# Performance work log

Measured on AMD Instinct MI355X. Metric: run time of the kernel, lower is better.

## Reference

```python
import jax, jax.numpy as jnp
import numpy as np

B, T, DIN, H, NOUT = 256, 512, 64, 512, 128


def setup_inputs() -> dict:
    key = jax.random.key(0)
    ks = jax.random.split(key, 11)
    s = 1.0 / np.sqrt(H)  # PyTorch GRU init scale
    inp = {"x": jax.random.normal(ks[0], (B, T, DIN), dtype=jnp.float32)}
    # layer 0 (input DIN), layer 1 (input H); gate order: r, z, n
    inp["w_ih0"] = jax.random.uniform(ks[1], (3 * H, DIN), minval=-s, maxval=s)
    inp["w_hh0"] = jax.random.uniform(ks[2], (3 * H, H), minval=-s, maxval=s)
    inp["b_ih0"] = jax.random.uniform(ks[3], (3 * H,), minval=-s, maxval=s)
    inp["b_hh0"] = jax.random.uniform(ks[4], (3 * H,), minval=-s, maxval=s)
    inp["w_ih1"] = jax.random.uniform(ks[5], (3 * H, H), minval=-s, maxval=s)
    inp["w_hh1"] = jax.random.uniform(ks[6], (3 * H, H), minval=-s, maxval=s)
    inp["b_ih1"] = jax.random.uniform(ks[7], (3 * H,), minval=-s, maxval=s)
    inp["b_hh1"] = jax.random.uniform(ks[8], (3 * H,), minval=-s, maxval=s)
    inp["w_fc"] = jax.random.uniform(ks[9], (NOUT, H), minval=-s, maxval=s)
    inp["b_fc"] = jax.random.uniform(ks[10], (NOUT,), minval=-s, maxval=s)
    return inp


def _gru_layer(x_seq, w_ih, w_hh, b_ih, b_hh):
    # x_seq: [B, T, Din] -> hidden trajectory [B, T, H]
    xg = jnp.einsum('btd,gd->btg', x_seq, w_ih) + b_ih  # [B, T, 3H], precomputed input gates
    h0 = jnp.zeros((x_seq.shape[0], w_hh.shape[1]), dtype=x_seq.dtype)

    def step(h, xg_t):
        hg = h @ w_hh.T + b_hh
        xr, xz, xn = jnp.split(xg_t, 3, axis=-1)
        hr, hz, hn = jnp.split(hg, 3, axis=-1)
        r = jax.nn.sigmoid(xr + hr)
        z = jax.nn.sigmoid(xz + hz)
        n = jnp.tanh(xn + r * hn)
        h_new = (1.0 - z) * n + z * h
        return h_new, h_new

    _, hs = jax.lax.scan(step, h0, jnp.swapaxes(xg, 0, 1))  # [T, B, H]
    return jnp.swapaxes(hs, 0, 1)


def reference(x, w_ih0, w_hh0, b_ih0, b_hh0, w_ih1, w_hh1, b_ih1, b_hh1, w_fc, b_fc):
    h1 = _gru_layer(x, w_ih0, w_hh0, b_ih0, b_hh0)   # [B, T, H]
    h2 = _gru_layer(h1, w_ih1, w_hh1, b_ih1, b_hh1)  # [B, T, H]
    last = h2[:, -1, :]                               # [B, H]
    return last @ w_fc.T + b_fc                       # [B, NOUT]
```

## Files before the change

### kernel.cpp

```cpp
#include <hip/hip_runtime.h>
#include <math.h>

typedef unsigned short u16;
typedef __attribute__((ext_vector_type(8))) short s8v;
typedef __attribute__((ext_vector_type(4))) float f4v;
typedef __attribute__((ext_vector_type(4))) int   i4v;

constexpr int kB    = 256;
constexpr int kT    = 512;
constexpr int kDIN  = 64;
constexpr int kH    = 512;
constexpr int kG3   = 1536;
constexpr int kNOUT = 128;
constexpr int kPlane = 8 * 2 * 16 * 512;
constexpr int kXStep = 16 * 2 * 512;

#define MFMA16 __builtin_amdgcn_mfma_f32_16x16x32_bf16

__device__ __forceinline__ u16 f2bf(float f) {
  union { float f; unsigned u; } v; v.f = f;
  unsigned r = (v.u + 0x7FFFu + ((v.u >> 16) & 1u)) >> 16;
  return (u16)r;
}
__device__ __forceinline__ float fsig(float x) {
  x = fminf(fmaxf(x, -30.f), 30.f);
  float e = __expf(-x);
  return __fdividef(1.f, 1.f + e);
}
__device__ __forceinline__ float ftanh(float x) {
  x = fminf(fmaxf(x, -15.f), 15.f);
  float e = __expf(-2.f * x);
  return __fdividef(1.f - e, 1.f + e);
}

__device__ __forceinline__ void load16_nw(const u16* base, i4v a[16]) {
  asm volatile(
      "global_load_dwordx4 %0, %16, off sc0 sc1\n\t"
      "global_load_dwordx4 %1, %16, off offset:1024 sc0 sc1\n\t"
      "global_load_dwordx4 %2, %16, off offset:2048 sc0 sc1\n\t"
      "global_load_dwordx4 %3, %16, off offset:3072 sc0 sc1\n\t"
      "global_load_dwordx4 %4, %17, off sc0 sc1\n\t"
      "global_load_dwordx4 %5, %17, off offset:1024 sc0 sc1\n\t"
      "global_load_dwordx4 %6, %17, off offset:2048 sc0 sc1\n\t"
      "global_load_dwordx4 %7, %17, off offset:3072 sc0 sc1\n\t"
      "global_load_dwordx4 %8, %18, off sc0 sc1\n\t"
      "global_load_dwordx4 %9, %18, off offset:1024 sc0 sc1\n\t"
      "global_load_dwordx4 %10, %18, off offset:2048 sc0 sc1\n\t"
      "global_load_dwordx4 %11, %18, off offset:3072 sc0 sc1\n\t"
      "global_load_dwordx4 %12, %19, off sc0 sc1\n\t"
      "global_load_dwordx4 %13, %19, off offset:1024 sc0 sc1\n\t"
      "global_load_dwordx4 %14, %19, off offset:2048 sc0 sc1\n\t"
      "global_load_dwordx4 %15, %19, off offset:3072 sc0 sc1"
      : "=&v"(a[0]), "=&v"(a[1]), "=&v"(a[2]), "=&v"(a[3]),
        "=&v"(a[4]), "=&v"(a[5]), "=&v"(a[6]), "=&v"(a[7]),
        "=&v"(a[8]), "=&v"(a[9]), "=&v"(a[10]), "=&v"(a[11]),
        "=&v"(a[12]), "=&v"(a[13]), "=&v"(a[14]), "=&v"(a[15])
      : "v"(base), "v"(base + 4 * 512), "v"(base + 8 * 512), "v"(base + 12 * 512)
      : "memory");
}

__device__ __forceinline__ void store_h_l0(
    u16* p0, u16* p1, u16* p2, u16* p3,
    u16* q0, u16* q1, u16* q2, u16* q3,
    unsigned v0, unsigned v1, unsigned v2, unsigned v3) {
  asm volatile(
      "global_store_short %0, %8, off sc0 sc1\n\t"
      "global_store_short %1, %9, off sc0 sc1\n\t"
      "global_store_short %2, %10, off sc0 sc1\n\t"
      "global_store_short %3, %11, off sc0 sc1\n\t"
      "global_store_short %4, %8, off\n\t"
      "global_store_short %5, %9, off\n\t"
      "global_store_short %6, %10, off\n\t"
      "global_store_short %7, %11, off\n\t"
      "s_waitcnt vmcnt(4)"
      :: "v"(p0), "v"(p1), "v"(p2), "v"(p3),
         "v"(q0), "v"(q1), "v"(q2), "v"(q3),
         "v"(v0), "v"(v1), "v"(v2), "v"(v3)
      : "memory");
}
__device__ __forceinline__ void store_h_l1(
    u16* p0, u16* p1, u16* p2, u16* p3,
    unsigned v0, unsigned v1, unsigned v2, unsigned v3) {
  asm volatile(
      "global_store_short %0, %4, off sc0 sc1\n\t"
      "global_store_short %1, %5, off sc0 sc1\n\t"
      "global_store_short %2, %6, off sc0 sc1\n\t"
      "global_store_short %3, %7, off sc0 sc1\n\t"
      "s_waitcnt vmcnt(0)"
      :: "v"(p0), "v"(p1), "v"(p2), "v"(p3),
         "v"(v0), "v"(v1), "v"(v2), "v"(v3)
      : "memory");
}

__global__ void build_wslab(const float* __restrict__ w, u16* __restrict__ d) {
  int idx  = blockIdx.x * 256 + threadIdx.x;
  int lane = idx & 63, fg = idx >> 6;
  int jt = fg / 96, f = fg % 96;
  int nt = f >> 4, kt = f & 15;
  int g = nt >> 1, u = nt & 1;
  int row = g * 512 + jt * 32 + u * 16 + (lane & 15);
  int k0  = kt * 32 + (lane >> 4) * 8;
  const float* src = w + (size_t)row * 512 + k0;
  u16* dst = d + ((size_t)fg) * 512 + lane * 8;
#pragma unroll
  for (int i = 0; i < 8; i++) dst[i] = f2bf(src[i]);
}

__global__ void build_wslab_ih0(const float* __restrict__ w, u16* __restrict__ d) {
  int idx  = blockIdx.x * 256 + threadIdx.x;
  int lane = idx & 63, fg = idx >> 6;
  int jt = fg / 12, f = fg % 12;
  int nt = f >> 1, kt = f & 1;
  int g = nt >> 1, u = nt & 1;
  int row = g * 512 + jt * 32 + u * 16 + (lane & 15);
  int k0  = kt * 32 + (lane >> 4) * 8;
  const float* src = w + (size_t)row * kDIN + k0;
  u16* dst = d + ((size_t)fg) * 512 + lane * 8;
#pragma unroll
  for (int i = 0; i < 8; i++) dst[i] = f2bf(src[i]);
}

__global__ void build_xplane(const float* __restrict__ x, u16* __restrict__ d) {
  int idx  = blockIdx.x * 256 + threadIdx.x;
  int lane = idx & 63, fg = idx >> 6;
  int kt = fg & 1, m = (fg >> 1) & 15, T = fg >> 5;
  int b  = m * 16 + (lane & 15);
  int k0 = kt * 32 + (lane >> 4) * 8;
  const float* src = x + ((size_t)b * kT + T) * kDIN + k0;
  u16* dst = d + ((size_t)fg) * 512 + lane * 8;
#pragma unroll
  for (int i = 0; i < 8; i++) dst[i] = f2bf(src[i]);
}

__global__ __launch_bounds__(256, 1)
void rec_fused(int c, int TC, int nc, unsigned bar_base16, unsigned* bar,
               const u16* __restrict__ xpl,
               const u16* __restrict__ slab0hh, const u16* __restrict__ slab0ih,
               const u16* __restrict__ slab1hh, const u16* __restrict__ slab1ih,
               const float* __restrict__ bih0, const float* __restrict__ bhh0,
               const float* __restrict__ bih1, const float* __restrict__ bhh1,
               u16* __restrict__ h1pl, u16* __restrict__ hbuf,
               float* __restrict__ carry) {
  __shared__ u16 ldsw[96 * 512];

  const int bid   = blockIdx.x;
  const int layer = bid >> 7;
  const int lb    = bid & 127;
  const int jt    = lb & 15, bt = lb >> 4;
  const int cc    = (layer == 0) ? c : c - 1;
  const bool active = (cc >= 0 && cc < nc);

  unsigned* mybar = bar + (size_t)(layer * 8 + bt) * 64;

  if (!active) {
    if (threadIdx.x == 0)
      __hip_atomic_fetch_add(mybar, (unsigned)TC, __ATOMIC_RELAXED,
                             __HIP_MEMORY_SCOPE_AGENT);
    return;
  }

  const int tid   = threadIdx.x;
  const int wv    = tid >> 6, lane = tid & 63;
  const int mt    = wv >> 1, u = wv & 1;
  const int jl    = lane & 15;
  const int jg    = jt * 32 + u * 16 + jl;
  const int mrow  = (lane >> 4) * 4;
  const int bbase = bt * 32 + mt * 16 + mrow;

  const size_t cons_off = ((size_t)((bt * 2 + mt) * 16)) * 512 + lane * 8;
  const size_t prod_off = ((size_t)((bt * 2 + mt) * 16 + jt)) * 512 +
                          (size_t)(16 * (u * 2 + (jl >> 3))) * 8 + (jl & 7);
  float* mycarry = carry + (size_t)layer * kB * kH;

  if (layer == 0) {
    s8v bh[3][16];
    {
      const u16* base = slab0hh + (size_t)jt * 96 * 512 + (size_t)lane * 8;
#pragma unroll
      for (int g = 0; g < 3; ++g)
#pragma unroll
        for (int kt = 0; kt < 16; ++kt)
          bh[g][kt] = *(const s8v*)(base + (size_t)((g * 2 + u) * 16 + kt) * 512);
    }
    s8v bx[3][2];
    {
      const u16* base = slab0ih + (size_t)jt * 12 * 512 + (size_t)lane * 8;
#pragma unroll
      for (int g = 0; g < 3; ++g)
#pragma unroll
        for (int kt = 0; kt < 2; ++kt)
          bx[g][kt] = *(const s8v*)(base + (size_t)((g * 2 + u) * 2 + kt) * 512);
    }
    const float br  = bih0[jg] + bhh0[jg];
    const float bz  = bih0[512 + jg] + bhh0[512 + jg];
    const float bni = bih0[1024 + jg], bnh = bhh0[1024 + jg];

    float hp[4];
#pragma unroll
    for (int r = 0; r < 4; ++r)
      hp[r] = mycarry[(size_t)(bbase + r) * 512 + jg];

    const size_t xoff = (size_t)((bt * 2 + mt) * 2) * 512 + (size_t)lane * 8;
    const u16* xb0 = xpl + (size_t)(cc * TC) * kXStep + xoff;
    s8v ax0 = *(const s8v*)xb0;
    s8v ax1 = *(const s8v*)(xb0 + 512);

    for (int t = 0; t < TC; ++t) {
      if (tid == 0) {
        unsigned tgt = bar_base16 + 16u * (unsigned)t;
        int guard = 0;
        while (__hip_atomic_load(mybar, __ATOMIC_RELAXED,
                                 __HIP_MEMORY_SCOPE_AGENT) < tgt
               && ++guard < (1 << 21))
          __builtin_amdgcn_s_sleep(1);
      }
      __syncthreads();

      i4v a[16];
      load16_nw(hbuf + (size_t)(t & 1) * kPlane + cons_off, a);

      const f4v z4 = {0.f, 0.f, 0.f, 0.f};
      f4v acc0, acc1, acc2, acc2x;
      acc0  = MFMA16(ax0, bx[0][0], z4, 0, 0, 0);
      acc0  = MFMA16(ax1, bx[0][1], acc0, 0, 0, 0);
      acc1  = MFMA16(ax0, bx[1][0], z4, 0, 0, 0);
      acc1  = MFMA16(ax1, bx[1][1], acc1, 0, 0, 0);
      acc2x = MFMA16(ax0, bx[2][0], z4, 0, 0, 0);
      acc2x = MFMA16(ax1, bx[2][1], acc2x, 0, 0, 0);
      acc2  = z4;
      asm volatile("s_waitcnt vmcnt(0)" ::: "memory");
      __builtin_amdgcn_sched_barrier(0);
#pragma unroll
      for (int kt = 0; kt < 16; ++kt) {
        const s8v av = __builtin_bit_cast(s8v, a[kt]);
        acc0 = MFMA16(av, bh[0][kt], acc0, 0, 0, 0);
        acc1 = MFMA16(av, bh[1][kt], acc1, 0, 0, 0);
        acc2 = MFMA16(av, bh[2][kt], acc2, 0, 0, 0);
      }

      unsigned hv[4];
#pragma unroll
      for (int r = 0; r < 4; ++r) {
        float rr = fsig(acc0[r] + br);
        float zz = fsig(acc1[r] + bz);
        float nn = ftanh(acc2x[r] + bni + rr * (acc2[r] + bnh));
        float hn = (1.f - zz) * nn + zz * hp[r];
        hp[r] = hn;
        hv[r] = f2bf(hn);
      }

      u16* pb = hbuf + (size_t)((t + 1) & 1) * kPlane + prod_off;
      u16* qb = h1pl + (size_t)((cc & 1) * TC + t) * kPlane + prod_off;
      store_h_l0(pb + (size_t)(mrow + 0) * 8, pb + (size_t)(mrow + 1) * 8,
                 pb + (size_t)(mrow + 2) * 8, pb + (size_t)(mrow + 3) * 8,
                 qb + (size_t)(mrow + 0) * 8, qb + (size_t)(mrow + 1) * 8,
                 qb + (size_t)(mrow + 2) * 8, qb + (size_t)(mrow + 3) * 8,
                 hv[0], hv[1], hv[2], hv[3]);
      __syncthreads();
      if (tid == 0)
        __hip_atomic_fetch_add(mybar, 1u, __ATOMIC_RELAXED,
                               __HIP_MEMORY_SCOPE_AGENT);
      if (t + 1 < TC) {
        const u16* xb = xpl + (size_t)(cc * TC + t + 1) * kXStep + xoff;
        ax0 = *(const s8v*)xb;
        ax1 = *(const s8v*)(xb + 512);
      }
    }
#pragma unroll
    for (int r = 0; r < 4; ++r)
      mycarry[(size_t)(bbase + r) * 512 + jg] = hp[r];
  } else {
    {
      const u16* src = slab1ih + (size_t)jt * 96 * 512;
      for (int i = tid; i < 96 * 512 / 8; i += 256)
        *(s8v*)&ldsw[i * 8] = *(const s8v*)&src[i * 8];
    }
    s8v bh[3][16];
    {
      const u16* base = slab1hh + (size_t)jt * 96 * 512 + (size_t)lane * 8;
#pragma unroll
      for (int g = 0; g < 3; ++g)
#pragma unroll
        for (int kt = 0; kt < 16; ++kt)
          bh[g][kt] = *(const s8v*)(base + (size_t)((g * 2 + u) * 16 + kt) * 512);
    }
    const float br  = bih1[jg] + bhh1[jg];
    const float bz  = bih1[512 + jg] + bhh1[512 + jg];
    const float bni = bih1[1024 + jg], bnh = bhh1[1024 + jg];

    float hp[4];
#pragma unroll
    for (int r = 0; r < 4; ++r)
      hp[r] = mycarry[(size_t)(bbase + r) * 512 + jg];

    const u16* h1base = h1pl + (size_t)((cc & 1) * TC) * kPlane + cons_off;
    i4v a1[16];
    load16_nw(h1base, a1);

    for (int t = 0; t < TC; ++t) {
      if (tid == 0) {
        unsigned tgt = bar_base16 + 16u * (unsigned)t;
        int guard = 0;
        while (__hip_atomic_load(mybar, __ATOMIC_RELAXED,
                                 __HIP_MEMORY_SCOPE_AGENT) < tgt
               && ++guard < (1 << 21))
          __builtin_amdgcn_s_sleep(1);
      }
      __syncthreads();

      i4v a2[16];
      load16_nw(hbuf + (size_t)(2 + (t & 1)) * kPlane + cons_off, a2);
      asm volatile("s_waitcnt vmcnt(16)" ::: "memory");
      __builtin_amdgcn_sched_barrier(0);

      const f4v z4 = {0.f, 0.f, 0.f, 0.f};
      f4v acc0 = z4, acc1 = z4, acc2 = z4, acc2x = z4;
#pragma unroll
      for (int kt = 0; kt < 16; ++kt) {
        const s8v b0 = *(const s8v*)&ldsw[(size_t)((0 + u) * 16 + kt) * 512 + lane * 8];
        const s8v b1 = *(const s8v*)&ldsw[(size_t)((2 + u) * 16 + kt) * 512 + lane * 8];
        const s8v b2 = *(const s8v*)&ldsw[(size_t)((4 + u) * 16 + kt) * 512 + lane * 8];
        const s8v av = __builtin_bit_cast(s8v, a1[kt]);
        acc0  = MFMA16(av, b0, acc0, 0, 0, 0);
        acc1  = MFMA16(av, b1, acc1, 0, 0, 0);
        acc2x = MFMA16(av, b2, acc2x, 0, 0, 0);
      }
      asm volatile("s_waitcnt vmcnt(0)" ::: "memory");
      __builtin_amdgcn_sched_barrier(0);
#pragma unroll
      for (int kt = 0; kt < 16; ++kt) {
        const s8v av = __builtin_bit_cast(s8v, a2[kt]);
        acc0 = MFMA16(av, bh[0][kt], acc0, 0, 0, 0);
        acc1 = MFMA16(av, bh[1][kt], acc1, 0, 0, 0);
        acc2 = MFMA16(av, bh[2][kt], acc2, 0, 0, 0);
      }

      unsigned hv[4];
#pragma unroll
      for (int r = 0; r < 4; ++r) {
        float rr = fsig(acc0[r] + br);
        float zz = fsig(acc1[r] + bz);
        float nn = ftanh(acc2x[r] + bni + rr * (acc2[r] + bnh));
        float hn = (1.f - zz) * nn + zz * hp[r];
        hp[r] = hn;
        hv[r] = f2bf(hn);
      }

      u16* pb = hbuf + (size_t)(2 + ((t + 1) & 1)) * kPlane + prod_off;
      store_h_l1(pb + (size_t)(mrow + 0) * 8, pb + (size_t)(mrow + 1) * 8,
                 pb + (size_t)(mrow + 2) * 8, pb + (size_t)(mrow + 3) * 8,
                 hv[0], hv[1], hv[2], hv[3]);
      if (t + 1 < TC)
        load16_nw(h1base + (size_t)(t + 1) * kPlane, a1);
      __syncthreads();
      if (tid == 0)
        __hip_atomic_fetch_add(mybar, 1u, __ATOMIC_RELAXED,
                               __HIP_MEMORY_SCOPE_AGENT);
    }
#pragma unroll
    for (int r = 0; r < 4; ++r)
      mycarry[(size_t)(bbase + r) * 512 + jg] = hp[r];
  }
}

__global__ __launch_bounds__(128)
void fc_kernel(const float* __restrict__ h, const float* __restrict__ wfc,
               const float* __restrict__ bfc, float* __restrict__ out) {
  const int b = blockIdx.x;
  const int n = threadIdx.x;
  const float* hrow = h + (size_t)b * kH;
  const float* wrow = wfc + (size_t)n * kH;
  float acc = 0.f;
#pragma unroll 4
  for (int k = 0; k < kH; k += 4) {
    const float4 hv = *(const float4*)&hrow[k];
    const float4 wv = *(const float4*)&wrow[k];
    acc = fmaf(hv.x, wv.x, acc); acc = fmaf(hv.y, wv.y, acc);
    acc = fmaf(hv.z, wv.z, acc); acc = fmaf(hv.w, wv.w, acc);
  }
  out[(size_t)b * kNOUT + n] = acc + bfc[n];
}

extern "C" void kernel_launch(void* const* d_in, const int* in_sizes, int n_in,
                              void* d_out, int out_size, void* d_ws, size_t ws_size,
                              hipStream_t stream) {
  const float* x     = (const float*)d_in[0];
  const float* w_ih0 = (const float*)d_in[1];
  const float* w_hh0 = (const float*)d_in[2];
  const float* b_ih0 = (const float*)d_in[3];
  const float* b_hh0 = (const float*)d_in[4];
  const float* w_ih1 = (const float*)d_in[5];
  const float* w_hh1 = (const float*)d_in[6];
  const float* b_ih1 = (const float*)d_in[7];
  const float* b_hh1 = (const float*)d_in[8];
  const float* w_fc  = (const float*)d_in[9];
  const float* b_fc  = (const float*)d_in[10];
  float* out = (float*)d_out;

  auto need = [](int tc) -> size_t {
    size_t s = 0;
    s += 3 * (size_t)kG3 * kH * 2;
    s += (size_t)kG3 * kDIN * 2;
    s += (size_t)kT * kXStep * 2;
    s += 2 * (size_t)tc * kPlane * 2;
    s += 4 * (size_t)kPlane * 2;
    s += 2 * (size_t)kB * kH * 4;
    s += 65536;
    return s;
  };
  int TC = 64;
  while (TC > 2 && need(TC) > ws_size) TC >>= 1;
  const int nc = kT / TC;

  char* p = (char*)d_ws;
  auto carve = [&](size_t bytes) {
    char* r = p; p += (bytes + 255) & ~(size_t)255; return r;
  };
  u16* slab0hh = (u16*)carve((size_t)kG3 * kH * 2);
  u16* slab1hh = (u16*)carve((size_t)kG3 * kH * 2);
  u16* slab1ih = (u16*)carve((size_t)kG3 * kH * 2);
  u16* slab0ih = (u16*)carve((size_t)kG3 * kDIN * 2);
  u16* xpl     = (u16*)carve((size_t)kT * kXStep * 2);
  u16* h1pl    = (u16*)carve(2 * (size_t)TC * kPlane * 2);
  u16* hbuf    = (u16*)carve(4 * (size_t)kPlane * 2);
  float* carry = (float*)carve(2 * (size_t)kB * kH * 4);
  unsigned* bar = (unsigned*)carve(32 * 64 * sizeof(unsigned));

  build_wslab<<<384, 256, 0, stream>>>(w_hh0, slab0hh);
  build_wslab<<<384, 256, 0, stream>>>(w_hh1, slab1hh);
  build_wslab<<<384, 256, 0, stream>>>(w_ih1, slab1ih);
  build_wslab_ih0<<<48, 256, 0, stream>>>(w_ih0, slab0ih);
  build_xplane<<<4096, 256, 0, stream>>>(x, xpl);
  hipMemsetAsync(hbuf, 0, 4 * (size_t)kPlane * 2 + 2 * (size_t)kB * kH * 4, stream);
  hipMemsetAsync(bar, 0, 32 * 64 * sizeof(unsigned), stream);

  for (int c = 0; c <= nc; ++c) {
    unsigned base16 = (unsigned)c * 16u * (unsigned)TC;
    rec_fused<<<dim3(256), dim3(256), 0, stream>>>(
        c, TC, nc, base16, bar, xpl,
        slab0hh, slab0ih, slab1hh, slab1ih,
        b_ih0, b_hh0, b_ih1, b_hh1,
        h1pl, hbuf, carry);
  }

  fc_kernel<<<dim3(kB), dim3(kNOUT), 0, stream>>>(
      carry + (size_t)kB * kH, w_fc, b_fc, out);
}
```

Measured before the change: 2.351 ms.

## Run both GRU layers in one persistent kernel with cross-layer flag sync

Replaces the chunked schedule (nc+1 launches, layer 1 lagging layer 0 by one chunk) with a single persistent launch. Layer 1 blocks now poll the layer-0 barrier counters so they trail layer 0 by only two timesteps. The full h1 trajectory is stored in a T-length buffer, and the layer-0 copies of h1 are written coherently (sc0 sc1) and waited on before signalling. This removes repeated launch and pipeline fill/drain costs and the carry save/restore between chunks. In exchange it adds extra polling, stronger store waits on layer 0, and more workspace.

```diff
diff --git a/kernel.cpp b/kernel.cpp
--- a/kernel.cpp
+++ b/kernel.cpp
@@ -59,7 +59,7 @@
       : "memory");
 }
 
-__device__ __forceinline__ void store_h_l0(
+__device__ __forceinline__ void store8c(
     u16* p0, u16* p1, u16* p2, u16* p3,
     u16* q0, u16* q1, u16* q2, u16* q3,
     unsigned v0, unsigned v1, unsigned v2, unsigned v3) {
@@ -68,11 +68,11 @@
       "global_store_short %1, %9, off sc0 sc1\n\t"
       "global_store_short %2, %10, off sc0 sc1\n\t"
       "global_store_short %3, %11, off sc0 sc1\n\t"
-      "global_store_short %4, %8, off\n\t"
-      "global_store_short %5, %9, off\n\t"
-      "global_store_short %6, %10, off\n\t"
-      "global_store_short %7, %11, off\n\t"
-      "s_waitcnt vmcnt(4)"
+      "global_store_short %4, %8, off sc0 sc1\n\t"
+      "global_store_short %5, %9, off sc0 sc1\n\t"
+      "global_store_short %6, %10, off sc0 sc1\n\t"
+      "global_store_short %7, %11, off sc0 sc1\n\t"
+      "s_waitcnt vmcnt(0)"
       :: "v"(p0), "v"(p1), "v"(p2), "v"(p3),
          "v"(q0), "v"(q1), "v"(q2), "v"(q3),
          "v"(v0), "v"(v1), "v"(v2), "v"(v3)
@@ -133,31 +133,23 @@
 }
 
 __global__ __launch_bounds__(256, 1)
-void rec_fused(int c, int TC, int nc, unsigned bar_base16, unsigned* bar,
-               const u16* __restrict__ xpl,
-               const u16* __restrict__ slab0hh, const u16* __restrict__ slab0ih,
-               const u16* __restrict__ slab1hh, const u16* __restrict__ slab1ih,
-               const float* __restrict__ bih0, const float* __restrict__ bhh0,
-               const float* __restrict__ bih1, const float* __restrict__ bhh1,
-               u16* __restrict__ h1pl, u16* __restrict__ hbuf,
-               float* __restrict__ carry) {
+void rec_all(unsigned* bar, const u16* __restrict__ xpl,
+             const u16* __restrict__ slab0hh, const u16* __restrict__ slab0ih,
+             const u16* __restrict__ slab1hh, const u16* __restrict__ slab1ih,
+             const float* __restrict__ bih0, const float* __restrict__ bhh0,
+             const float* __restrict__ bih1, const float* __restrict__ bhh1,
+             u16* __restrict__ h1pl, u16* __restrict__ hbuf,
+             float* __restrict__ carry) {
   __shared__ u16 ldsw[96 * 512];
 
   const int bid   = blockIdx.x;
   const int layer = bid >> 7;
   const int lb    = bid & 127;
   const int jt    = lb & 15, bt = lb >> 4;
-  const int cc    = (layer == 0) ? c : c - 1;
-  const bool active = (cc >= 0 && cc < nc);
-
-  unsigned* mybar = bar + (size_t)(layer * 8 + bt) * 64;
-
-  if (!active) {
-    if (threadIdx.x == 0)
-      __hip_atomic_fetch_add(mybar, (unsigned)TC, __ATOMIC_RELAXED,
-                             __HIP_MEMORY_SCOPE_AGENT);
-    return;
-  }
+
+  unsigned* barL0 = bar + (size_t)bt * 64;
+  unsigned* barL1 = bar + (size_t)(8 + bt) * 64;
+  unsigned* mybar = layer ? barL1 : barL0;
 
   const int tid   = threadIdx.x;
   const int wv    = tid >> 6, lane = tid & 63;
@@ -170,7 +162,6 @@
   const size_t cons_off = ((size_t)((bt * 2 + mt) * 16)) * 512 + lane * 8;
   const size_t prod_off = ((size_t)((bt * 2 + mt) * 16 + jt)) * 512 +
                           (size_t)(16 * (u * 2 + (jl >> 3))) * 8 + (jl & 7);
-  float* mycarry = carry + (size_t)layer * kB * kH;
 
   if (layer == 0) {
     s8v bh[3][16];
@@ -194,22 +185,17 @@
     const float br  = bih0[jg] + bhh0[jg];
     const float bz  = bih0[512 + jg] + bhh0[512 + jg];
     const float bni = bih0[1024 + jg], bnh = bhh0[1024 + jg];
-
-    float hp[4];
-#pragma unroll
-    for (int r = 0; r < 4; ++r)
-      hp[r] = mycarry[(size_t)(bbase + r) * 512 + jg];
+    float hp[4] = {0.f, 0.f, 0.f, 0.f};
 
     const size_t xoff = (size_t)((bt * 2 + mt) * 2) * 512 + (size_t)lane * 8;
-    const u16* xb0 = xpl + (size_t)(cc * TC) * kXStep + xoff;
-    s8v ax0 = *(const s8v*)xb0;
-    s8v ax1 = *(const s8v*)(xb0 + 512);
-
-    for (int t = 0; t < TC; ++t) {
-      if (tid == 0) {
-        unsigned tgt = bar_base16 + 16u * (unsigned)t;
+    s8v ax0 = *(const s8v*)(xpl + xoff);
+    s8v ax1 = *(const s8v*)(xpl + xoff + 512);
+
+    for (int t = 0; t < kT; ++t) {
+      if (tid == 0 && t) {
+        unsigned tgt = 16u * (unsigned)t;
         int guard = 0;
-        while (__hip_atomic_load(mybar, __ATOMIC_RELAXED,
+        while (__hip_atomic_load(barL0, __ATOMIC_RELAXED,
                                  __HIP_MEMORY_SCOPE_AGENT) < tgt
                && ++guard < (1 << 21))
           __builtin_amdgcn_s_sleep(1);
@@ -250,25 +236,22 @@
       }
 
       u16* pb = hbuf + (size_t)((t + 1) & 1) * kPlane + prod_off;
-      u16* qb = h1pl + (size_t)((cc & 1) * TC + t) * kPlane + prod_off;
-      store_h_l0(pb + (size_t)(mrow + 0) * 8, pb + (size_t)(mrow + 1) * 8,
-                 pb + (size_t)(mrow + 2) * 8, pb + (size_t)(mrow + 3) * 8,
-                 qb + (size_t)(mrow + 0) * 8, qb + (size_t)(mrow + 1) * 8,
-                 qb + (size_t)(mrow + 2) * 8, qb + (size_t)(mrow + 3) * 8,
-                 hv[0], hv[1], hv[2], hv[3]);
+      u16* qb = h1pl + (size_t)t * kPlane + prod_off;
+      store8c(pb + (size_t)(mrow + 0) * 8, pb + (size_t)(mrow + 1) * 8,
+              pb + (size_t)(mrow + 2) * 8, pb + (size_t)(mrow + 3) * 8,
+              qb + (size_t)(mrow + 0) * 8, qb + (size_t)(mrow + 1) * 8,
+              qb + (size_t)(mrow + 2) * 8, qb + (size_t)(mrow + 3) * 8,
+              hv[0], hv[1], hv[2], hv[3]);
       __syncthreads();
       if (tid == 0)
-        __hip_atomic_fetch_add(mybar, 1u, __ATOMIC_RELAXED,
+        __hip_atomic_fetch_add(barL0, 1u, __ATOMIC_RELAXED,
                                __HIP_MEMORY_SCOPE_AGENT);
-      if (t + 1 < TC) {
-        const u16* xb = xpl + (size_t)(cc * TC + t + 1) * kXStep + xoff;
+      if (t + 1 < kT) {
+        const u16* xb = xpl + (size_t)(t + 1) * kXStep + xoff;
         ax0 = *(const s8v*)xb;
         ax1 = *(const s8v*)(xb + 512);
       }
     }
-#pragma unroll
-    for (int r = 0; r < 4; ++r)
-      mycarry[(size_t)(bbase + r) * 512 + jg] = hp[r];
   } else {
     {
       const u16* src = slab1ih + (size_t)jt * 96 * 512;
@@ -287,29 +270,33 @@
     const float br  = bih1[jg] + bhh1[jg];
     const float bz  = bih1[512 + jg] + bhh1[512 + jg];
     const float bni = bih1[1024 + jg], bnh = bhh1[1024 + jg];
-
-    float hp[4];
-#pragma unroll
-    for (int r = 0; r < 4; ++r)
-      hp[r] = mycarry[(size_t)(bbase + r) * 512 + jg];
-
-    const u16* h1base = h1pl + (size_t)((cc & 1) * TC) * kPlane + cons_off;
+    float hp[4] = {0.f, 0.f, 0.f, 0.f};
+
+    const u16* h1base = h1pl + cons_off;
     i4v a1[16];
-    load16_nw(h1base, a1);
-
-    for (int t = 0; t < TC; ++t) {
-      if (tid == 0) {
-        unsigned tgt = bar_base16 + 16u * (unsigned)t;
+
+    for (int s = 0; s < kT; ++s) {
+      if (tid == 0 && s) {
+        unsigned tgt = 16u * (unsigned)s;
         int guard = 0;
-        while (__hip_atomic_load(mybar, __ATOMIC_RELAXED,
+        while (__hip_atomic_load(barL1, __ATOMIC_RELAXED,
                                  __HIP_MEMORY_SCOPE_AGENT) < tgt
                && ++guard < (1 << 21))
           __builtin_amdgcn_s_sleep(1);
+      } else if (tid == 64) {
+        unsigned tgt = 16u * (unsigned)((s + 2 <= kT) ? (s + 2) : kT);
+        int guard = 0;
+        while (__hip_atomic_load(barL0, __ATOMIC_RELAXED,
+                                 __HIP_MEMORY_SCOPE_AGENT) < tgt
+               && ++guard < (1 << 21))
+          __builtin_amdgcn_s_sleep(1);
       }
       __syncthreads();
 
+      if (s == 0) load16_nw(h1base, a1);
+
       i4v a2[16];
-      load16_nw(hbuf + (size_t)(2 + (t & 1)) * kPlane + cons_off, a2);
+      load16_nw(hbuf + (size_t)(2 + (s & 1)) * kPlane + cons_off, a2);
       asm volatile("s_waitcnt vmcnt(16)" ::: "memory");
       __builtin_amdgcn_sched_barrier(0);
 
@@ -346,20 +333,21 @@
         hv[r] = f2bf(hn);
       }
 
-      u16* pb = hbuf + (size_t)(2 + ((t + 1) & 1)) * kPlane + prod_off;
+      u16* pb = hbuf + (size_t)(2 + ((s + 1) & 1)) * kPlane + prod_off;
       store_h_l1(pb + (size_t)(mrow + 0) * 8, pb + (size_t)(mrow + 1) * 8,
                  pb + (size_t)(mrow + 2) * 8, pb + (size_t)(mrow + 3) * 8,
                  hv[0], hv[1], hv[2], hv[3]);
-      if (t + 1 < TC)
-        load16_nw(h1base + (size_t)(t + 1) * kPlane, a1);
       __syncthreads();
       if (tid == 0)
-        __hip_atomic_fetch_add(mybar, 1u, __ATOMIC_RELAXED,
+        __hip_atomic_fetch_add(barL1, 1u, __ATOMIC_RELAXED,
                                __HIP_MEMORY_SCOPE_AGENT);
-    }
+      if (s + 1 < kT)
+        load16_nw(h1base + (size_t)(s + 1) * kPlane, a1);
+    }
+
 #pragma unroll
     for (int r = 0; r < 4; ++r)
-      mycarry[(size_t)(bbase + r) * 512 + jg] = hp[r];
+      carry[(size_t)(bbase + r) * 512 + jg] = hp[r];
   }
 }
 
@@ -397,21 +385,6 @@
   const float* b_fc  = (const float*)d_in[10];
   float* out = (float*)d_out;
 
-  auto need = [](int tc) -> size_t {
-    size_t s = 0;
-    s += 3 * (size_t)kG3 * kH * 2;
-    s += (size_t)kG3 * kDIN * 2;
-    s += (size_t)kT * kXStep * 2;
-    s += 2 * (size_t)tc * kPlane * 2;
-    s += 4 * (size_t)kPlane * 2;
-    s += 2 * (size_t)kB * kH * 4;
-    s += 65536;
-    return s;
-  };
-  int TC = 64;
-  while (TC > 2 && need(TC) > ws_size) TC >>= 1;
-  const int nc = kT / TC;
-
   char* p = (char*)d_ws;
   auto carve = [&](size_t bytes) {
     char* r = p; p += (bytes + 255) & ~(size_t)255; return r;
@@ -421,28 +394,22 @@
   u16* slab1ih = (u16*)carve((size_t)kG3 * kH * 2);
   u16* slab0ih = (u16*)carve((size_t)kG3 * kDIN * 2);
   u16* xpl     = (u16*)carve((size_t)kT * kXStep * 2);
-  u16* h1pl    = (u16*)carve(2 * (size_t)TC * kPlane * 2);
+  u16* h1pl    = (u16*)carve((size_t)kT * kPlane * 2);
   u16* hbuf    = (u16*)carve(4 * (size_t)kPlane * 2);
-  float* carry = (float*)carve(2 * (size_t)kB * kH * 4);
-  unsigned* bar = (unsigned*)carve(32 * 64 * sizeof(unsigned));
+  float* carry = (float*)carve((size_t)kB * kH * 4);
+  unsigned* bar = (unsigned*)carve(16 * 64 * sizeof(unsigned));
 
   build_wslab<<<384, 256, 0, stream>>>(w_hh0, slab0hh);
   build_wslab<<<384, 256, 0, stream>>>(w_hh1, slab1hh);
   build_wslab<<<384, 256, 0, stream>>>(w_ih1, slab1ih);
   build_wslab_ih0<<<48, 256, 0, stream>>>(w_ih0, slab0ih);
   build_xplane<<<4096, 256, 0, stream>>>(x, xpl);
-  hipMemsetAsync(hbuf, 0, 4 * (size_t)kPlane * 2 + 2 * (size_t)kB * kH * 4, stream);
-  hipMemsetAsync(bar, 0, 32 * 64 * sizeof(unsigned), stream);
-
-  for (int c = 0; c <= nc; ++c) {
-    unsigned base16 = (unsigned)c * 16u * (unsigned)TC;
-    rec_fused<<<dim3(256), dim3(256), 0, stream>>>(
-        c, TC, nc, base16, bar, xpl,
-        slab0hh, slab0ih, slab1hh, slab1ih,
-        b_ih0, b_hh0, b_ih1, b_hh1,
-        h1pl, hbuf, carry);
-  }
-
-  fc_kernel<<<dim3(kB), dim3(kNOUT), 0, stream>>>(
-      carry + (size_t)kB * kH, w_fc, b_fc, out);
-}
+  hipMemsetAsync(hbuf, 0, 4 * (size_t)kPlane * 2, stream);
+  hipMemsetAsync(bar, 0, 16 * 64 * sizeof(unsigned), stream);
+
+  rec_all<<<dim3(256), dim3(256), 0, stream>>>(
+      bar, xpl, slab0hh, slab0ih, slab1hh, slab1ih,
+      b_ih0, b_hh0, b_ih1, b_hh1, h1pl, hbuf, carry);
+
+  fc_kernel<<<dim3(kB), dim3(kNOUT), 0, stream>>>(carry, w_fc, b_fc, out);
+}
```

After: 2.217 ms. 1.06x faster.
